# Optimization experiments

Hardware: AMD Instinct MI355X
Metric: run time of the kernel (lower is better)

Reference implementation:

```python
import jax, jax.numpy as jnp
from jax import lax
import numpy as np

N, I, H, B, T = 16, 128, 128, 32, 512  # n lstms, input_size, hidden_size, batch, seq_len


def setup_inputs() -> dict:
    key = jax.random.key(0)
    k0, k1, k2, k3, k4 = jax.random.split(key, 5)
    s = 1.0 / np.sqrt(H)  # PyTorch LSTM init scale U(-1/sqrt(H), 1/sqrt(H)); normal*s is fine numerically
    x = jax.random.normal(k0, (B, T, N * I), dtype=jnp.float32)
    W_ih = jax.random.normal(k1, (N, 4 * H, I), dtype=jnp.float32) * s
    W_hh = jax.random.normal(k2, (N, 4 * H, H), dtype=jnp.float32) * s
    b_ih = jax.random.normal(k3, (N, 4 * H), dtype=jnp.float32) * s
    b_hh = jax.random.normal(k4, (N, 4 * H), dtype=jnp.float32) * s
    return {"x": x, "W_ih": W_ih, "W_hh": W_hh, "b_ih": b_ih, "b_hh": b_hh}


def reference(x, W_ih, W_hh, b_ih, b_hh):
    """WideLSTM fused forward: N independent single-layer unidirectional LSTMs,
    hx=None (zero initial state), batch_first output [B, T, N*H], (h_n, c_n) [1, B, N*H].
    PyTorch gate order: i, f, g, o."""
    Bx, Tx, _ = x.shape
    n = W_ih.shape[0]
    h = W_hh.shape[-1]
    xs = x.reshape(Bx, Tx, n, -1).transpose(1, 0, 2, 3)  # [T, B, N, I]
    # Precompute input contribution + biases for all timesteps at once (one big GEMM)
    x_proj = jnp.einsum('tbni,ngi->tbng', xs, W_ih) + (b_ih + b_hh)  # [T, B, N, 4H]

    def step(carry, xp):
        hprev, cprev = carry
        z = xp + jnp.einsum('bnh,ngh->bng', hprev, W_hh)  # [B, N, 4H]
        i_g, f_g, g_g, o_g = jnp.split(z, 4, axis=-1)
        i_g = jax.nn.sigmoid(i_g)
        f_g = jax.nn.sigmoid(f_g)
        g_g = jnp.tanh(g_g)
        o_g = jax.nn.sigmoid(o_g)
        c = f_g * cprev + i_g * g_g
        hnew = o_g * jnp.tanh(c)
        return (hnew, c), hnew

    h0 = jnp.zeros((Bx, n, h), dtype=x.dtype)
    c0 = jnp.zeros((Bx, n, h), dtype=x.dtype)
    (h_n, c_n), hs = lax.scan(step, (h0, c0), x_proj)
    output = hs.transpose(1, 0, 2, 3).reshape(Bx, Tx, n * h)  # [B, T, N*H]
    h_n = h_n.reshape(1, Bx, n * h)  # [num_layers*num_dir=1, B, N*H]
    c_n = c_n.reshape(1, Bx, n * h)
    return output, h_n, c_n
```

## Files before the change

### kernel.cpp

```cpp
#include <hip/hip_runtime.h>

#define N_LSTM 16
#define ISZ 128
#define HSZ 128
#define BSZ 32
#define TSZ 512
#define G4H 512
#define XROW (N_LSTM * ISZ)
#define OROW (N_LSTM * HSZ)

typedef __attribute__((ext_vector_type(8))) short s16x8;
typedef __attribute__((ext_vector_type(4))) float f32x4;

#define LOG2E 1.4426950408889634f

static __device__ __forceinline__ unsigned short f2bf(float f) {
    unsigned int u = __builtin_bit_cast(unsigned int, f);
    u += 0x7fffu + ((u >> 16) & 1u);
    return (unsigned short)(u >> 16);
}

static __device__ __forceinline__ float fexp2(float x) {
#if __has_builtin(__builtin_amdgcn_exp2f)
    return __builtin_amdgcn_exp2f(x);
#else
    return __expf(x * 0.6931471805599453f);
#endif
}

static __device__ __forceinline__ void barrier_lgkm() {
    __builtin_amdgcn_sched_barrier(0);
    asm volatile("s_waitcnt lgkmcnt(0)" ::: "memory");
    __builtin_amdgcn_s_barrier();
    __builtin_amdgcn_sched_barrier(0);
}

__global__ void x_to_frag(const float* __restrict__ x, int4* __restrict__ xf) {
    const unsigned G = blockIdx.x * 256 + threadIdx.x;
    const int ln = G & 63;
    const int kt = (G >> 6) & 3;
    const int wg = (G >> 8) & 31;
    const int t  = G >> 13;
    const int lm = ln & 15, lq = ln >> 4;
    const int n  = wg >> 1;
    const int b0 = (wg & 1) * 16;
    const float* src = x + (size_t)(b0 + lm) * (TSZ * XROW) + (size_t)t * XROW
                         + n * ISZ + kt * 32 + lq * 8;
    float4 a = *(const float4*)src;
    float4 b = *(const float4*)(src + 4);
    s16x8 f;
    f[0] = (short)f2bf(a.x); f[1] = (short)f2bf(a.y);
    f[2] = (short)f2bf(a.z); f[3] = (short)f2bf(a.w);
    f[4] = (short)f2bf(b.x); f[5] = (short)f2bf(b.y);
    f[6] = (short)f2bf(b.z); f[7] = (short)f2bf(b.w);
    xf[G] = __builtin_bit_cast(int4, f);
}

template <int PRE>
__global__ __launch_bounds__(512, 2) void widelstm_fused(
    const float* __restrict__ x, const int4* __restrict__ xf,
    const float* __restrict__ Wih, const float* __restrict__ Whh,
    const float* __restrict__ bih, const float* __restrict__ bhh,
    float* __restrict__ out)
{
    __shared__ __align__(16) unsigned short xbuf[2][16][136];
    __shared__ __align__(16) unsigned short hbuf[2][16][136];

    const int tid = threadIdx.x;
    const int wv  = tid >> 6;
    const int ln  = tid & 63;
    const int lm  = ln & 15;
    const int lq  = ln >> 4;
    const int n    = blockIdx.x >> 1;
    const int half = blockIdx.x & 1;
    const int b0   = half * 16;
    const int grp = (wv ^ (wv >> 2)) & 1;

    const float gsc[4] = {-LOG2E, -LOG2E, -2.f * LOG2E, -LOG2E};
    s16x8 wih[4][4], whh[4][4];
    f32x4 biasv[4];
    #pragma unroll
    for (int g = 0; g < 4; ++g) {
        const int col = g * 128 + wv * 16 + lm;
        const float s = gsc[g];
        const float bb = (bih[n * G4H + col] + bhh[n * G4H + col]) * s;
        biasv[g] = (f32x4){bb, bb, bb, bb};
        #pragma unroll
        for (int kt = 0; kt < 4; ++kt) {
            const float* pi = Wih + ((size_t)n * G4H + col) * ISZ + kt * 32 + lq * 8;
            const float* ph = Whh + ((size_t)n * G4H + col) * HSZ + kt * 32 + lq * 8;
            s16x8 a, b;
            #pragma unroll
            for (int j = 0; j < 8; ++j) {
                a[j] = (short)f2bf(pi[j] * s);
                b[j] = (short)f2bf(ph[j] * s);
            }
            wih[g][kt] = a;
            whh[g][kt] = b;
        }
    }

    for (int i = tid; i < 16 * 136; i += 512)
        ((unsigned short*)hbuf[0])[i] = 0;

    const int sr = tid >> 5;
    const int sc = (tid & 31) * 4;
    const float* xrow = x + (size_t)(b0 + sr) * TSZ * XROW + n * ISZ + sc;
    const int4* xfb = xf + (size_t)blockIdx.x * 256 + ln;

    float4 xr;
    s16x8 xra, xrb, xrc, xrd;
    f32x4 xacc[4];

    if constexpr (PRE) {
        s16x8 c0 = __builtin_bit_cast(s16x8, xfb[0]);
        s16x8 c1 = __builtin_bit_cast(s16x8, xfb[64]);
        s16x8 c2 = __builtin_bit_cast(s16x8, xfb[128]);
        s16x8 c3 = __builtin_bit_cast(s16x8, xfb[192]);
        #pragma unroll
        for (int g = 0; g < 4; ++g)
            xacc[g] = __builtin_amdgcn_mfma_f32_16x16x32_bf16(c0, wih[g][0], biasv[g], 0, 0, 0);
        #pragma unroll
        for (int g = 0; g < 4; ++g)
            xacc[g] = __builtin_amdgcn_mfma_f32_16x16x32_bf16(c1, wih[g][1], xacc[g], 0, 0, 0);
        #pragma unroll
        for (int g = 0; g < 4; ++g)
            xacc[g] = __builtin_amdgcn_mfma_f32_16x16x32_bf16(c2, wih[g][2], xacc[g], 0, 0, 0);
        #pragma unroll
        for (int g = 0; g < 4; ++g)
            xacc[g] = __builtin_amdgcn_mfma_f32_16x16x32_bf16(c3, wih[g][3], xacc[g], 0, 0, 0);
        xra = __builtin_bit_cast(s16x8, xfb[8192]);
        xrb = __builtin_bit_cast(s16x8, xfb[8192 + 64]);
        xrc = __builtin_bit_cast(s16x8, xfb[8192 + 128]);
        xrd = __builtin_bit_cast(s16x8, xfb[8192 + 192]);
    } else {
        xr = *(const float4*)(xrow);
        unsigned int lo = (unsigned int)f2bf(xr.x) | ((unsigned int)f2bf(xr.y) << 16);
        unsigned int hi = (unsigned int)f2bf(xr.z) | ((unsigned int)f2bf(xr.w) << 16);
        *(uint2*)&xbuf[0][sr][sc] = make_uint2(lo, hi);
        barrier_lgkm();
        #pragma unroll
        for (int kt = 0; kt < 4; ++kt) {
            s16x8 axk = *(const s16x8*)&xbuf[0][lm][kt * 32 + lq * 8];
            #pragma unroll
            for (int g = 0; g < 4; ++g)
                xacc[g] = __builtin_amdgcn_mfma_f32_16x16x32_bf16(
                    axk, wih[g][kt], kt == 0 ? biasv[g] : xacc[g], 0, 0, 0);
        }
        xr = *(const float4*)(xrow + (size_t)XROW);
    }

    float cprev[4] = {0.f, 0.f, 0.f, 0.f};
    float hlast[4] = {0.f, 0.f, 0.f, 0.f};
    const int ocol = n * HSZ + wv * 16 + lm;

    float* po0 = out + (size_t)(b0 + lq * 4 + 0) * TSZ * OROW + ocol;
    float* po1 = out + (size_t)(b0 + lq * 4 + 1) * TSZ * OROW + ocol;
    float* po2 = out + (size_t)(b0 + lq * 4 + 2) * TSZ * OROW + ocol;
    float* po3 = out + (size_t)(b0 + lq * 4 + 3) * TSZ * OROW + ocol;

#define PH_X(T_)                                                                            \
    if ((T_) + 1 < TSZ) {                                                                   \
        _Pragma("unroll")                                                                   \
        for (int g = 0; g < 4; ++g)                                                         \
            xacc[g] = __builtin_amdgcn_mfma_f32_16x16x32_bf16(xra, wih[g][0], biasv[g], 0, 0, 0); \
        _Pragma("unroll")                                                                   \
        for (int g = 0; g < 4; ++g)                                                         \
            xacc[g] = __builtin_amdgcn_mfma_f32_16x16x32_bf16(xrb, wih[g][1], xacc[g], 0, 0, 0); \
        _Pragma("unroll")                                                                   \
        for (int g = 0; g < 4; ++g)                                                         \
            xacc[g] = __builtin_amdgcn_mfma_f32_16x16x32_bf16(xrc, wih[g][2], xacc[g], 0, 0, 0); \
        _Pragma("unroll")                                                                   \
        for (int g = 0; g < 4; ++g)                                                         \
            xacc[g] = __builtin_amdgcn_mfma_f32_16x16x32_bf16(xrd, wih[g][3], xacc[g], 0, 0, 0); \
        if ((T_) + 2 < TSZ) {                                                               \
            const int4* p = xfb + (size_t)((T_) + 2) * 8192;                                \
            xra = __builtin_bit_cast(s16x8, p[0]);                                          \
            xrb = __builtin_bit_cast(s16x8, p[64]);                                         \
            xrc = __builtin_bit_cast(s16x8, p[128]);                                        \
            xrd = __builtin_bit_cast(s16x8, p[192]);                                        \
        }                                                                                   \
    }

#define PH_EPI(NXT_)                                                                        \
    _Pragma("unroll")                                                                       \
    for (int r = 0; r < 4; ++r) {                                                           \
        float ei = fexp2(hacc[0][r]);                                                       \
        float ef = fexp2(hacc[1][r]);                                                       \
        float eg = fexp2(fminf(hacc[2][r], 80.f));                                          \
        float eo = fexp2(hacc[3][r]);                                                       \
        float fv = __builtin_amdgcn_rcpf(1.f + ef);                                         \
        float ig = (1.f - eg) * __builtin_amdgcn_rcpf((1.f + ei) * (1.f + eg));             \
        float c  = fv * cprev[r] + ig;                                                      \
        cprev[r] = c;                                                                       \
        float ec = fexp2(fminf(c * (-2.f * LOG2E), 80.f));                                  \
        float hv = (1.f - ec) * __builtin_amdgcn_rcpf((1.f + eo) * (1.f + ec));             \
        hlast[r] = hv;                                                                      \
        hbuf[NXT_][lq * 4 + r][wv * 16 + lm] = f2bf(hv);                                    \
        if (r == 0) { *po0 = hv; po0 += OROW; }                                             \
        if (r == 1) { *po1 = hv; po1 += OROW; }                                             \
        if (r == 2) { *po2 = hv; po2 += OROW; }                                             \
        if (r == 3) { *po3 = hv; po3 += OROW; }                                             \
    }

#define LSTM_STEP(T_, CUR_, NXT_)                                                           \
    {                                                                                       \
        const int t_ = (T_);                                                                \
        if constexpr (!PRE) {                                                               \
            if (t_ + 1 < TSZ) {                                                             \
                unsigned int lo = (unsigned int)f2bf(xr.x) | ((unsigned int)f2bf(xr.y) << 16); \
                unsigned int hi = (unsigned int)f2bf(xr.z) | ((unsigned int)f2bf(xr.w) << 16); \
                *(uint2*)&xbuf[NXT_][sr][sc] = make_uint2(lo, hi);                          \
            }                                                                               \
        }                                                                                   \
        barrier_lgkm();                  \
        s16x8 ah0 = *(const s16x8*)&hbuf[CUR_][lm][0 * 32 + lq * 8];                        \
        s16x8 ah1 = *(const s16x8*)&hbuf[CUR_][lm][1 * 32 + lq * 8];                        \
        s16x8 ah2 = *(const s16x8*)&hbuf[CUR_][lm][2 * 32 + lq * 8];                        \
        s16x8 ah3 = *(const s16x8*)&hbuf[CUR_][lm][3 * 32 + lq * 8];                        \
        if constexpr (!PRE) {                                                               \
            if (t_ + 2 < TSZ) xr = *(const float4*)(xrow + (size_t)(t_ + 2) * XROW);        \
        }                                                                                   \
        f32x4 hacc[4];                                                                      \
        _Pragma("unroll")                                                                   \
        for (int g = 0; g < 4; ++g)                                                         \
            hacc[g] = __builtin_amdgcn_mfma_f32_16x16x32_bf16(ah0, whh[g][0], xacc[g], 0, 0, 0); \
        _Pragma("unroll")                                                                   \
        for (int g = 0; g < 4; ++g)                                                         \
            hacc[g] = __builtin_amdgcn_mfma_f32_16x16x32_bf16(ah1, whh[g][1], hacc[g], 0, 0, 0); \
        _Pragma("unroll")                                                                   \
        for (int g = 0; g < 4; ++g)                                                         \
            hacc[g] = __builtin_amdgcn_mfma_f32_16x16x32_bf16(ah2, whh[g][2], hacc[g], 0, 0, 0); \
        _Pragma("unroll")                                                                   \
        for (int g = 0; g < 4; ++g)                                                         \
            hacc[g] = __builtin_amdgcn_mfma_f32_16x16x32_bf16(ah3, whh[g][3], hacc[g], 0, 0, 0); \
        if constexpr (PRE) {                                                                \
            if (grp == 0) {                                                                 \
                PH_X(t_);                                                                   \
                __builtin_amdgcn_sched_barrier(0);                                          \
                PH_EPI(NXT_);                                                               \
            } else {                                                                        \
                PH_EPI(NXT_);                                                               \
                __builtin_amdgcn_sched_barrier(0);                                          \
                PH_X(t_);                                                                   \
            }                                                                               \
        } else {                                                                            \
            if (t_ + 1 < TSZ) {                                                             \
                _Pragma("unroll")                                                           \
                for (int kt = 0; kt < 4; ++kt) {                                            \
                    s16x8 axk = *(const s16x8*)&xbuf[NXT_][lm][kt * 32 + lq * 8];           \
                    _Pragma("unroll")                                                       \
                    for (int g = 0; g < 4; ++g)                                             \
                        xacc[g] = __builtin_amdgcn_mfma_f32_16x16x32_bf16(                  \
                            axk, wih[g][kt], kt == 0 ? biasv[g] : xacc[g], 0, 0, 0);        \
                }                                                                           \
            }                                                                               \
            PH_EPI(NXT_);                                                                   \
        }                                                                                   \
    }

    for (int t = 0; t < TSZ; t += 2) {
        LSTM_STEP(t, 0, 1);
        LSTM_STEP(t + 1, 1, 0);
    }
#undef LSTM_STEP
#undef PH_X
#undef PH_EPI

    const size_t hn_off = (size_t)BSZ * TSZ * OROW;
    const size_t cn_off = hn_off + (size_t)BSZ * OROW;
    #pragma unroll
    for (int r = 0; r < 4; ++r) {
        const int row = lq * 4 + r;
        const size_t idx = (size_t)(b0 + row) * OROW + ocol;
        out[hn_off + idx] = hlast[r];
        out[cn_off + idx] = cprev[r];
    }
}

extern "C" void kernel_launch(void* const* d_in, const int* in_sizes, int n_in,
                              void* d_out, int out_size, void* d_ws, size_t ws_size,
                              hipStream_t stream) {
    const float* x   = (const float*)d_in[0];
    const float* Wih = (const float*)d_in[1];
    const float* Whh = (const float*)d_in[2];
    const float* bih = (const float*)d_in[3];
    const float* bhh = (const float*)d_in[4];
    float* out = (float*)d_out;

    const size_t need = (size_t)TSZ * 32 * 4 * 64 * 16;
    if (d_ws != nullptr && ws_size >= need) {
        int4* xfrag = (int4*)d_ws;
        x_to_frag<<<dim3(16384), dim3(256), 0, stream>>>(x, xfrag);
        widelstm_fused<1><<<dim3(32), dim3(512), 0, stream>>>(x, xfrag, Wih, Whh, bih, bhh, out);
    } else {
        widelstm_fused<0><<<dim3(32), dim3(512), 0, stream>>>(x, nullptr, Wih, Whh, bih, bhh, out);
    }
}
```

Baseline: 752.7 us.

## Precompute input projection in a parallel GEMM kernel before the recurrent scan

Adds an xp_gemm kernel that computes the input projection plus bias for all timesteps on a 32x8 grid and writes it in fp32 fragment layout to the workspace. A new recurrent kernel then only does the hidden-state MFMAs each step and prefetches the precomputed gate pre-activations two steps ahead. This takes the per-step W_ih MFMAs off the serial critical path, at the cost of a large fp32 workspace write and read (about 134 MB). The old fused kernel loses its wave-group phase staggering and remains as a fallback.

Measured after the change: 932.3 us. 1.24x slower.

```diff
diff --git a/kernel.cpp b/kernel.cpp
--- a/kernel.cpp
+++ b/kernel.cpp
@@ -33,6 +33,190 @@
     asm volatile("s_waitcnt lgkmcnt(0)" ::: "memory");
     __builtin_amdgcn_s_barrier();
     __builtin_amdgcn_sched_barrier(0);
+}
+
+__global__ __launch_bounds__(512, 2) void xp_gemm(
+    const float* __restrict__ x, const float* __restrict__ Wih,
+    const float* __restrict__ bih, const float* __restrict__ bhh,
+    float* __restrict__ xp)
+{
+    const int tid = threadIdx.x;
+    const int wv  = tid >> 6;
+    const int ln  = tid & 63;
+    const int lm  = ln & 15;
+    const int lq  = ln >> 4;
+    const int wg  = blockIdx.x;
+    const int tc  = blockIdx.y;
+    const int n   = wg >> 1;
+    const int b0  = (wg & 1) * 16;
+
+    const float gsc[4] = {-LOG2E, -LOG2E, -2.f * LOG2E, -LOG2E};
+    s16x8 wih[4][4];
+    f32x4 biasv[4];
+    #pragma unroll
+    for (int g = 0; g < 4; ++g) {
+        const int col = g * 128 + wv * 16 + lm;
+        const float s = gsc[g];
+        const float bb = (bih[n * G4H + col] + bhh[n * G4H + col]) * s;
+        biasv[g] = (f32x4){bb, bb, bb, bb};
+        #pragma unroll
+        for (int kt = 0; kt < 4; ++kt) {
+            const float* pi = Wih + ((size_t)n * G4H + col) * ISZ + kt * 32 + lq * 8;
+            s16x8 a;
+            #pragma unroll
+            for (int j = 0; j < 8; ++j) a[j] = (short)f2bf(pi[j] * s);
+            wih[g][kt] = a;
+        }
+    }
+
+    const float* xbase = x + (size_t)(b0 + lm) * (TSZ * XROW) + n * ISZ + lq * 8;
+    float* xpo = xp + (size_t)(wg * 8 + wv) * 1024 + ln * 4;
+
+    #pragma unroll 2
+    for (int tt = 0; tt < 64; ++tt) {
+        const int t = tc * 64 + tt;
+        const float* xr = xbase + (size_t)t * XROW;
+        s16x8 fr[4];
+        #pragma unroll
+        for (int kt = 0; kt < 4; ++kt) {
+            float4 a = *(const float4*)(xr + kt * 32);
+            float4 b = *(const float4*)(xr + kt * 32 + 4);
+            s16x8 f;
+            f[0] = (short)f2bf(a.x); f[1] = (short)f2bf(a.y);
+            f[2] = (short)f2bf(a.z); f[3] = (short)f2bf(a.w);
+            f[4] = (short)f2bf(b.x); f[5] = (short)f2bf(b.y);
+            f[6] = (short)f2bf(b.z); f[7] = (short)f2bf(b.w);
+            fr[kt] = f;
+        }
+        f32x4 acc[4];
+        #pragma unroll
+        for (int g = 0; g < 4; ++g) acc[g] = biasv[g];
+        #pragma unroll
+        for (int kt = 0; kt < 4; ++kt) {
+            #pragma unroll
+            for (int g = 0; g < 4; ++g)
+                acc[g] = __builtin_amdgcn_mfma_f32_16x16x32_bf16(fr[kt], wih[g][kt], acc[g], 0, 0, 0);
+        }
+        float* o = xpo + (size_t)t * 262144;
+        #pragma unroll
+        for (int g = 0; g < 4; ++g)
+            *(f32x4*)(o + g * 256) = acc[g];
+    }
+}
+
+__global__ __launch_bounds__(512, 2) void widelstm_rec_xp(
+    const float* __restrict__ xp, const float* __restrict__ Whh,
+    float* __restrict__ out)
+{
+    __shared__ __align__(16) unsigned short hbuf[2][16][136];
+
+    const int tid = threadIdx.x;
+    const int wv  = tid >> 6;
+    const int ln  = tid & 63;
+    const int lm  = ln & 15;
+    const int lq  = ln >> 4;
+    const int n    = blockIdx.x >> 1;
+    const int half = blockIdx.x & 1;
+    const int b0   = half * 16;
+
+    const float gsc[4] = {-LOG2E, -LOG2E, -2.f * LOG2E, -LOG2E};
+    s16x8 whh[4][4];
+    #pragma unroll
+    for (int g = 0; g < 4; ++g) {
+        const int col = g * 128 + wv * 16 + lm;
+        const float s = gsc[g];
+        #pragma unroll
+        for (int kt = 0; kt < 4; ++kt) {
+            const float* ph = Whh + ((size_t)n * G4H + col) * HSZ + kt * 32 + lq * 8;
+            s16x8 b;
+            #pragma unroll
+            for (int j = 0; j < 8; ++j) b[j] = (short)f2bf(ph[j] * s);
+            whh[g][kt] = b;
+        }
+    }
+
+    for (int i = tid; i < 16 * 136; i += 512)
+        ((unsigned short*)hbuf[0])[i] = 0;
+
+    const float* xq = xp + (size_t)(blockIdx.x * 8 + wv) * 1024 + ln * 4;
+
+    f32x4 pA[4], pB[4];
+    #pragma unroll
+    for (int g = 0; g < 4; ++g) pA[g] = *(const f32x4*)(xq + g * 256);
+    #pragma unroll
+    for (int g = 0; g < 4; ++g) pB[g] = *(const f32x4*)(xq + 262144 + g * 256);
+
+    float cprev[4] = {0.f, 0.f, 0.f, 0.f};
+    float hlast[4] = {0.f, 0.f, 0.f, 0.f};
+    const int ocol = n * HSZ + wv * 16 + lm;
+
+    float* po0 = out + (size_t)(b0 + lq * 4 + 0) * TSZ * OROW + ocol;
+    float* po1 = out + (size_t)(b0 + lq * 4 + 1) * TSZ * OROW + ocol;
+    float* po2 = out + (size_t)(b0 + lq * 4 + 2) * TSZ * OROW + ocol;
+    float* po3 = out + (size_t)(b0 + lq * 4 + 3) * TSZ * OROW + ocol;
+
+#define XP_STEP(T_, CUR_, NXT_, PC_, PN_)                                                   \
+    {                                                                                       \
+        const int t_ = (T_);                                                                \
+        barrier_lgkm();                                      \
+        s16x8 ah0 = *(const s16x8*)&hbuf[CUR_][lm][0 * 32 + lq * 8];                        \
+        s16x8 ah1 = *(const s16x8*)&hbuf[CUR_][lm][1 * 32 + lq * 8];                        \
+        s16x8 ah2 = *(const s16x8*)&hbuf[CUR_][lm][2 * 32 + lq * 8];                        \
+        s16x8 ah3 = *(const s16x8*)&hbuf[CUR_][lm][3 * 32 + lq * 8];                        \
+        f32x4 hacc[4];                                                                      \
+        _Pragma("unroll")                                                                   \
+        for (int g = 0; g < 4; ++g)                                                         \
+            hacc[g] = __builtin_amdgcn_mfma_f32_16x16x32_bf16(ah0, whh[g][0], PC_[g], 0, 0, 0); \
+        _Pragma("unroll")                                                                   \
+        for (int g = 0; g < 4; ++g)                                                         \
+            hacc[g] = __builtin_amdgcn_mfma_f32_16x16x32_bf16(ah1, whh[g][1], hacc[g], 0, 0, 0); \
+        _Pragma("unroll")                                                                   \
+        for (int g = 0; g < 4; ++g)                                                         \
+            hacc[g] = __builtin_amdgcn_mfma_f32_16x16x32_bf16(ah2, whh[g][2], hacc[g], 0, 0, 0); \
+        _Pragma("unroll")                                                                   \
+        for (int g = 0; g < 4; ++g)                                                         \
+            hacc[g] = __builtin_amdgcn_mfma_f32_16x16x32_bf16(ah3, whh[g][3], hacc[g], 0, 0, 0); \
+        if (t_ + 2 < TSZ) {               \
+            const float* p = xq + (size_t)(t_ + 2) * 262144;                                \
+            _Pragma("unroll")                                                               \
+            for (int g = 0; g < 4; ++g) PC_[g] = *(const f32x4*)(p + g * 256);              \
+        }                                                                                   \
+        _Pragma("unroll")                                                                   \
+        for (int r = 0; r < 4; ++r) {                                                       \
+            float ei = fexp2(hacc[0][r]);                                                   \
+            float ef = fexp2(hacc[1][r]);                                                   \
+            float eg = fexp2(fminf(hacc[2][r], 80.f));                                      \
+            float eo = fexp2(hacc[3][r]);                                                   \
+            float fv = __builtin_amdgcn_rcpf(1.f + ef);                                     \
+            float ig = (1.f - eg) * __builtin_amdgcn_rcpf((1.f + ei) * (1.f + eg));         \
+            float c  = fv * cprev[r] + ig;                                                  \
+            cprev[r] = c;                                                                   \
+            float ec = fexp2(fminf(c * (-2.f * LOG2E), 80.f));                              \
+            float hv = (1.f - ec) * __builtin_amdgcn_rcpf((1.f + eo) * (1.f + ec));         \
+            hlast[r] = hv;                                                                  \
+            hbuf[NXT_][lq * 4 + r][wv * 16 + lm] = f2bf(hv);                                \
+            if (r == 0) { *po0 = hv; po0 += OROW; }                                         \
+            if (r == 1) { *po1 = hv; po1 += OROW; }                                         \
+            if (r == 2) { *po2 = hv; po2 += OROW; }                                         \
+            if (r == 3) { *po3 = hv; po3 += OROW; }                                         \
+        }                                                                                   \
+    }
+
+    for (int t = 0; t < TSZ; t += 2) {
+        XP_STEP(t, 0, 1, pA, pB);
+        XP_STEP(t + 1, 1, 0, pB, pA);
+    }
+#undef XP_STEP
+
+    const size_t hn_off = (size_t)BSZ * TSZ * OROW;
+    const size_t cn_off = hn_off + (size_t)BSZ * OROW;
+    #pragma unroll
+    for (int r = 0; r < 4; ++r) {
+        const int row = lq * 4 + r;
+        const size_t idx = (size_t)(b0 + row) * OROW + ocol;
+        out[hn_off + idx] = hlast[r];
+        out[cn_off + idx] = cprev[r];
+    }
 }
 
 __global__ void x_to_frag(const float* __restrict__ x, int4* __restrict__ xf) {
@@ -74,7 +258,6 @@
     const int n    = blockIdx.x >> 1;
     const int half = blockIdx.x & 1;
     const int b0   = half * 16;
-    const int grp = (wv ^ (wv >> 2)) & 1;
 
     const float gsc[4] = {-LOG2E, -LOG2E, -2.f * LOG2E, -LOG2E};
     s16x8 wih[4][4], whh[4][4];
@@ -159,50 +342,6 @@
     float* po2 = out + (size_t)(b0 + lq * 4 + 2) * TSZ * OROW + ocol;
     float* po3 = out + (size_t)(b0 + lq * 4 + 3) * TSZ * OROW + ocol;
 
-#define PH_X(T_)                                                                            \
-    if ((T_) + 1 < TSZ) {                                                                   \
-        _Pragma("unroll")                                                                   \
-        for (int g = 0; g < 4; ++g)                                                         \
-            xacc[g] = __builtin_amdgcn_mfma_f32_16x16x32_bf16(xra, wih[g][0], biasv[g], 0, 0, 0); \
-        _Pragma("unroll")                                                                   \
-        for (int g = 0; g < 4; ++g)                                                         \
-            xacc[g] = __builtin_amdgcn_mfma_f32_16x16x32_bf16(xrb, wih[g][1], xacc[g], 0, 0, 0); \
-        _Pragma("unroll")                                                                   \
-        for (int g = 0; g < 4; ++g)                                                         \
-            xacc[g] = __builtin_amdgcn_mfma_f32_16x16x32_bf16(xrc, wih[g][2], xacc[g], 0, 0, 0); \
-        _Pragma("unroll")                                                                   \
-        for (int g = 0; g < 4; ++g)                                                         \
-            xacc[g] = __builtin_amdgcn_mfma_f32_16x16x32_bf16(xrd, wih[g][3], xacc[g], 0, 0, 0); \
-        if ((T_) + 2 < TSZ) {                                                               \
-            const int4* p = xfb + (size_t)((T_) + 2) * 8192;                                \
-            xra = __builtin_bit_cast(s16x8, p[0]);                                          \
-            xrb = __builtin_bit_cast(s16x8, p[64]);                                         \
-            xrc = __builtin_bit_cast(s16x8, p[128]);                                        \
-            xrd = __builtin_bit_cast(s16x8, p[192]);                                        \
-        }                                                                                   \
-    }
-
-#define PH_EPI(NXT_)                                                                        \
-    _Pragma("unroll")                                                                       \
-    for (int r = 0; r < 4; ++r) {                                                           \
-        float ei = fexp2(hacc[0][r]);                                                       \
-        float ef = fexp2(hacc[1][r]);                                                       \
-        float eg = fexp2(fminf(hacc[2][r], 80.f));                                          \
-        float eo = fexp2(hacc[3][r]);                                                       \
-        float fv = __builtin_amdgcn_rcpf(1.f + ef);                                         \
-        float ig = (1.f - eg) * __builtin_amdgcn_rcpf((1.f + ei) * (1.f + eg));             \
-        float c  = fv * cprev[r] + ig;                                                      \
-        cprev[r] = c;                                                                       \
-        float ec = fexp2(fminf(c * (-2.f * LOG2E), 80.f));                                  \
-        float hv = (1.f - ec) * __builtin_amdgcn_rcpf((1.f + eo) * (1.f + ec));             \
-        hlast[r] = hv;                                                                      \
-        hbuf[NXT_][lq * 4 + r][wv * 16 + lm] = f2bf(hv);                                    \
-        if (r == 0) { *po0 = hv; po0 += OROW; }                                             \
-        if (r == 1) { *po1 = hv; po1 += OROW; }                                             \
-        if (r == 2) { *po2 = hv; po2 += OROW; }                                             \
-        if (r == 3) { *po3 = hv; po3 += OROW; }                                             \
-    }
-
 #define LSTM_STEP(T_, CUR_, NXT_)                                                           \
     {                                                                                       \
         const int t_ = (T_);                                                                \
@@ -213,7 +352,7 @@
                 *(uint2*)&xbuf[NXT_][sr][sc] = make_uint2(lo, hi);                          \
             }                                                                               \
         }                                                                                   \
-        barrier_lgkm();                  \
+        barrier_lgkm();                                                                     \
         s16x8 ah0 = *(const s16x8*)&hbuf[CUR_][lm][0 * 32 + lq * 8];                        \
         s16x8 ah1 = *(const s16x8*)&hbuf[CUR_][lm][1 * 32 + lq * 8];                        \
         s16x8 ah2 = *(const s16x8*)&hbuf[CUR_][lm][2 * 32 + lq * 8];                        \
@@ -234,18 +373,28 @@
         _Pragma("unroll")                                                                   \
         for (int g = 0; g < 4; ++g)                                                         \
             hacc[g] = __builtin_amdgcn_mfma_f32_16x16x32_bf16(ah3, whh[g][3], hacc[g], 0, 0, 0); \
-        if constexpr (PRE) {                                                                \
-            if (grp == 0) {                                                                 \
-                PH_X(t_);                                                                   \
-                __builtin_amdgcn_sched_barrier(0);                                          \
-                PH_EPI(NXT_);                                                               \
+        if (t_ + 1 < TSZ) {                                                                 \
+            if constexpr (PRE) {                                                            \
+                _Pragma("unroll")                                                           \
+                for (int g = 0; g < 4; ++g)                                                 \
+                    xacc[g] = __builtin_amdgcn_mfma_f32_16x16x32_bf16(xra, wih[g][0], biasv[g], 0, 0, 0); \
+                _Pragma("unroll")                                                           \
+                for (int g = 0; g < 4; ++g)                                                 \
+                    xacc[g] = __builtin_amdgcn_mfma_f32_16x16x32_bf16(xrb, wih[g][1], xacc[g], 0, 0, 0); \
+                _Pragma("unroll")                                                           \
+                for (int g = 0; g < 4; ++g)                                                 \
+                    xacc[g] = __builtin_amdgcn_mfma_f32_16x16x32_bf16(xrc, wih[g][2], xacc[g], 0, 0, 0); \
+                _Pragma("unroll")                                                           \
+                for (int g = 0; g < 4; ++g)                                                 \
+                    xacc[g] = __builtin_amdgcn_mfma_f32_16x16x32_bf16(xrd, wih[g][3], xacc[g], 0, 0, 0); \
+                if (t_ + 2 < TSZ) {                                                         \
+                    const int4* p = xfb + (size_t)(t_ + 2) * 8192;                          \
+                    xra = __builtin_bit_cast(s16x8, p[0]);                                  \
+                    xrb = __builtin_bit_cast(s16x8, p[64]);                                 \
+                    xrc = __builtin_bit_cast(s16x8, p[128]);                                \
+                    xrd = __builtin_bit_cast(s16x8, p[192]);                                \
+                }                                                                           \
             } else {                                                                        \
-                PH_EPI(NXT_);                                                               \
-                __builtin_amdgcn_sched_barrier(0);                                          \
-                PH_X(t_);                                                                   \
-            }                                                                               \
-        } else {                                                                            \
-            if (t_ + 1 < TSZ) {                                                             \
                 _Pragma("unroll")                                                           \
                 for (int kt = 0; kt < 4; ++kt) {                                            \
                     s16x8 axk = *(const s16x8*)&xbuf[NXT_][lm][kt * 32 + lq * 8];           \
@@ -255,7 +404,25 @@
                             axk, wih[g][kt], kt == 0 ? biasv[g] : xacc[g], 0, 0, 0);        \
                 }                                                                           \
             }                                                                               \
-            PH_EPI(NXT_);                                                                   \
+        }                                                                                   \
+        _Pragma("unroll")                                                                   \
+        for (int r = 0; r < 4; ++r) {                                                       \
+            float ei = fexp2(hacc[0][r]);                                                   \
+            float ef = fexp2(hacc[1][r]);                                                   \
+            float eg = fexp2(fminf(hacc[2][r], 80.f));                                      \
+            float eo = fexp2(hacc[3][r]);                                                   \
+            float fv = __builtin_amdgcn_rcpf(1.f + ef);                                     \
+            float ig = (1.f - eg) * __builtin_amdgcn_rcpf((1.f + ei) * (1.f + eg));         \
+            float c  = fv * cprev[r] + ig;                                                  \
+            cprev[r] = c;                                                                   \
+            float ec = fexp2(fminf(c * (-2.f * LOG2E), 80.f));                              \
+            float hv = (1.f - ec) * __builtin_amdgcn_rcpf((1.f + eo) * (1.f + ec));         \
+            hlast[r] = hv;                                                                  \
+            hbuf[NXT_][lq * 4 + r][wv * 16 + lm] = f2bf(hv);                                \
+            if (r == 0) { *po0 = hv; po0 += OROW; }                                         \
+            if (r == 1) { *po1 = hv; po1 += OROW; }                                         \
+            if (r == 2) { *po2 = hv; po2 += OROW; }                                         \
+            if (r == 3) { *po3 = hv; po3 += OROW; }                                         \
         }                                                                                   \
     }
 
@@ -264,8 +431,6 @@
         LSTM_STEP(t + 1, 1, 0);
     }
 #undef LSTM_STEP
-#undef PH_X
-#undef PH_EPI
 
     const size_t hn_off = (size_t)BSZ * TSZ * OROW;
     const size_t cn_off = hn_off + (size_t)BSZ * OROW;
@@ -288,8 +453,13 @@
     const float* bhh = (const float*)d_in[4];
     float* out = (float*)d_out;
 
-    const size_t need = (size_t)TSZ * 32 * 4 * 64 * 16;
-    if (d_ws != nullptr && ws_size >= need) {
+    const size_t needXP = (size_t)TSZ * 32 * 8 * 4 * 256 * 4;
+    const size_t needFR = (size_t)TSZ * 32 * 4 * 64 * 16;
+    if (d_ws != nullptr && ws_size >= needXP) {
+        float* xp = (float*)d_ws;
+        xp_gemm<<<dim3(32, 8), dim3(512), 0, stream>>>(x, Wih, bih, bhh, xp);
+        widelstm_rec_xp<<<dim3(32), dim3(512), 0, stream>>>(xp, Whh, out);
+    } else if (d_ws != nullptr && ws_size >= needFR) {
         int4* xfrag = (int4*)d_ws;
         x_to_frag<<<dim3(16384), dim3(256), 0, stream>>>(x, xfrag);
         widelstm_fused<1><<<dim3(32), dim3(512), 0, stream>>>(x, xfrag, Wih, Whh, bih, bhh, out);
```

## Double-buffer input-projection accumulators and issue next-step x MFMAs before recurrent MFMAs

Applied to the files above, without the earlier changes.

The recurrent step now computes the next timestep's input projection into a second accumulator set (ping-pong xaccA/xaccB) before the h·W_hh MFMAs. This replaces the wave-group split that ordered x-projection and epilogue differently per wave. The goal is to fill the MFMA pipe while waiting on the h dependency chain. The epilogue is reformulated to use one reciprocal for the cell update instead of two. Launch bounds drop to 1 block per CU, which gives more registers at the cost of occupancy hints.

Result: faster. 726.6 us (-3.5%).

```diff
diff --git a/kernel.cpp b/kernel.cpp
--- a/kernel.cpp
+++ b/kernel.cpp
@@ -57,7 +57,7 @@
 }
 
 template <int PRE>
-__global__ __launch_bounds__(512, 2) void widelstm_fused(
+__global__ __launch_bounds__(512, 1) void widelstm_fused(
     const float* __restrict__ x, const int4* __restrict__ xf,
     const float* __restrict__ Wih, const float* __restrict__ Whh,
     const float* __restrict__ bih, const float* __restrict__ bhh,
@@ -74,7 +74,6 @@
     const int n    = blockIdx.x >> 1;
     const int half = blockIdx.x & 1;
     const int b0   = half * 16;
-    const int grp = (wv ^ (wv >> 2)) & 1;
 
     const float gsc[4] = {-LOG2E, -LOG2E, -2.f * LOG2E, -LOG2E};
     s16x8 wih[4][4], whh[4][4];
@@ -110,7 +109,7 @@
 
     float4 xr;
     s16x8 xra, xrb, xrc, xrd;
-    f32x4 xacc[4];
+    f32x4 xaccA[4], xaccB[4];
 
     if constexpr (PRE) {
         s16x8 c0 = __builtin_bit_cast(s16x8, xfb[0]);
@@ -119,16 +118,16 @@
         s16x8 c3 = __builtin_bit_cast(s16x8, xfb[192]);
         #pragma unroll
         for (int g = 0; g < 4; ++g)
-            xacc[g] = __builtin_amdgcn_mfma_f32_16x16x32_bf16(c0, wih[g][0], biasv[g], 0, 0, 0);
+            xaccA[g] = __builtin_amdgcn_mfma_f32_16x16x32_bf16(c0, wih[g][0], biasv[g], 0, 0, 0);
         #pragma unroll
         for (int g = 0; g < 4; ++g)
-            xacc[g] = __builtin_amdgcn_mfma_f32_16x16x32_bf16(c1, wih[g][1], xacc[g], 0, 0, 0);
+            xaccA[g] = __builtin_amdgcn_mfma_f32_16x16x32_bf16(c1, wih[g][1], xaccA[g], 0, 0, 0);
         #pragma unroll
         for (int g = 0; g < 4; ++g)
-            xacc[g] = __builtin_amdgcn_mfma_f32_16x16x32_bf16(c2, wih[g][2], xacc[g], 0, 0, 0);
+            xaccA[g] = __builtin_amdgcn_mfma_f32_16x16x32_bf16(c2, wih[g][2], xaccA[g], 0, 0, 0);
         #pragma unroll
         for (int g = 0; g < 4; ++g)
-            xacc[g] = __builtin_amdgcn_mfma_f32_16x16x32_bf16(c3, wih[g][3], xacc[g], 0, 0, 0);
+            xaccA[g] = __builtin_amdgcn_mfma_f32_16x16x32_bf16(c3, wih[g][3], xaccA[g], 0, 0, 0);
         xra = __builtin_bit_cast(s16x8, xfb[8192]);
         xrb = __builtin_bit_cast(s16x8, xfb[8192 + 64]);
         xrc = __builtin_bit_cast(s16x8, xfb[8192 + 128]);
@@ -144,8 +143,8 @@
             s16x8 axk = *(const s16x8*)&xbuf[0][lm][kt * 32 + lq * 8];
             #pragma unroll
             for (int g = 0; g < 4; ++g)
-                xacc[g] = __builtin_amdgcn_mfma_f32_16x16x32_bf16(
-                    axk, wih[g][kt], kt == 0 ? biasv[g] : xacc[g], 0, 0, 0);
+                xaccA[g] = __builtin_amdgcn_mfma_f32_16x16x32_bf16(
+                    axk, wih[g][kt], kt == 0 ? biasv[g] : xaccA[g], 0, 0, 0);
         }
         xr = *(const float4*)(xrow + (size_t)XROW);
     }
@@ -158,29 +157,6 @@
     float* po1 = out + (size_t)(b0 + lq * 4 + 1) * TSZ * OROW + ocol;
     float* po2 = out + (size_t)(b0 + lq * 4 + 2) * TSZ * OROW + ocol;
     float* po3 = out + (size_t)(b0 + lq * 4 + 3) * TSZ * OROW + ocol;
-
-#define PH_X(T_)                                                                            \
-    if ((T_) + 1 < TSZ) {                                                                   \
-        _Pragma("unroll")                                                                   \
-        for (int g = 0; g < 4; ++g)                                                         \
-            xacc[g] = __builtin_amdgcn_mfma_f32_16x16x32_bf16(xra, wih[g][0], biasv[g], 0, 0, 0); \
-        _Pragma("unroll")                                                                   \
-        for (int g = 0; g < 4; ++g)                                                         \
-            xacc[g] = __builtin_amdgcn_mfma_f32_16x16x32_bf16(xrb, wih[g][1], xacc[g], 0, 0, 0); \
-        _Pragma("unroll")                                                                   \
-        for (int g = 0; g < 4; ++g)                                                         \
-            xacc[g] = __builtin_amdgcn_mfma_f32_16x16x32_bf16(xrc, wih[g][2], xacc[g], 0, 0, 0); \
-        _Pragma("unroll")                                                                   \
-        for (int g = 0; g < 4; ++g)                                                         \
-            xacc[g] = __builtin_amdgcn_mfma_f32_16x16x32_bf16(xrd, wih[g][3], xacc[g], 0, 0, 0); \
-        if ((T_) + 2 < TSZ) {                                                               \
-            const int4* p = xfb + (size_t)((T_) + 2) * 8192;                                \
-            xra = __builtin_bit_cast(s16x8, p[0]);                                          \
-            xrb = __builtin_bit_cast(s16x8, p[64]);                                         \
-            xrc = __builtin_bit_cast(s16x8, p[128]);                                        \
-            xrd = __builtin_bit_cast(s16x8, p[192]);                                        \
-        }                                                                                   \
-    }
 
 #define PH_EPI(NXT_)                                                                        \
     _Pragma("unroll")                                                                       \
@@ -189,9 +165,10 @@
         float ef = fexp2(hacc[1][r]);                                                       \
         float eg = fexp2(fminf(hacc[2][r], 80.f));                                          \
         float eo = fexp2(hacc[3][r]);                                                       \
-        float fv = __builtin_amdgcn_rcpf(1.f + ef);                                         \
-        float ig = (1.f - eg) * __builtin_amdgcn_rcpf((1.f + ei) * (1.f + eg));             \
-        float c  = fv * cprev[r] + ig;                                                      \
+        float af = 1.f + ef;                                                                \
+        float p1 = (1.f + ei) * (1.f + eg);                                                 \
+        float num = cprev[r] * p1 + (1.f - eg) * af;                                        \
+        float c   = num * __builtin_amdgcn_rcpf(af * p1);                                   \
         cprev[r] = c;                                                                       \
         float ec = fexp2(fminf(c * (-2.f * LOG2E), 80.f));                                  \
         float hv = (1.f - ec) * __builtin_amdgcn_rcpf((1.f + eo) * (1.f + ec));             \
@@ -203,28 +180,40 @@
         if (r == 3) { *po3 = hv; po3 += OROW; }                                             \
     }
 
-#define LSTM_STEP(T_, CUR_, NXT_)                                                           \
+    if constexpr (PRE) {
+#define STEP_P(T_, CUR_, NXT_, XC_, XN_)                                                    \
     {                                                                                       \
         const int t_ = (T_);                                                                \
-        if constexpr (!PRE) {                                                               \
-            if (t_ + 1 < TSZ) {                                                             \
-                unsigned int lo = (unsigned int)f2bf(xr.x) | ((unsigned int)f2bf(xr.y) << 16); \
-                unsigned int hi = (unsigned int)f2bf(xr.z) | ((unsigned int)f2bf(xr.w) << 16); \
-                *(uint2*)&xbuf[NXT_][sr][sc] = make_uint2(lo, hi);                          \
-            }                                                                               \
-        }                                                                                   \
-        barrier_lgkm();                  \
+        barrier_lgkm();                                      \
         s16x8 ah0 = *(const s16x8*)&hbuf[CUR_][lm][0 * 32 + lq * 8];                        \
         s16x8 ah1 = *(const s16x8*)&hbuf[CUR_][lm][1 * 32 + lq * 8];                        \
         s16x8 ah2 = *(const s16x8*)&hbuf[CUR_][lm][2 * 32 + lq * 8];                        \
         s16x8 ah3 = *(const s16x8*)&hbuf[CUR_][lm][3 * 32 + lq * 8];                        \
-        if constexpr (!PRE) {                                                               \
-            if (t_ + 2 < TSZ) xr = *(const float4*)(xrow + (size_t)(t_ + 2) * XROW);        \
+        if (t_ + 1 < TSZ) {               \
+            _Pragma("unroll")                                                               \
+            for (int g = 0; g < 4; ++g)                                                     \
+                XN_[g] = __builtin_amdgcn_mfma_f32_16x16x32_bf16(xra, wih[g][0], biasv[g], 0, 0, 0); \
+            _Pragma("unroll")                                                               \
+            for (int g = 0; g < 4; ++g)                                                     \
+                XN_[g] = __builtin_amdgcn_mfma_f32_16x16x32_bf16(xrb, wih[g][1], XN_[g], 0, 0, 0); \
+            _Pragma("unroll")                                                               \
+            for (int g = 0; g < 4; ++g)                                                     \
+                XN_[g] = __builtin_amdgcn_mfma_f32_16x16x32_bf16(xrc, wih[g][2], XN_[g], 0, 0, 0); \
+            _Pragma("unroll")                                                               \
+            for (int g = 0; g < 4; ++g)                                                     \
+                XN_[g] = __builtin_amdgcn_mfma_f32_16x16x32_bf16(xrd, wih[g][3], XN_[g], 0, 0, 0); \
+            if (t_ + 2 < TSZ) {                                 \
+                const int4* p = xfb + (size_t)(t_ + 2) * 8192;                              \
+                xra = __builtin_bit_cast(s16x8, p[0]);                                      \
+                xrb = __builtin_bit_cast(s16x8, p[64]);                                     \
+                xrc = __builtin_bit_cast(s16x8, p[128]);                                    \
+                xrd = __builtin_bit_cast(s16x8, p[192]);                                    \
+            }                                                                               \
         }                                                                                   \
         f32x4 hacc[4];                                                                      \
         _Pragma("unroll")                                                                   \
         for (int g = 0; g < 4; ++g)                                                         \
-            hacc[g] = __builtin_amdgcn_mfma_f32_16x16x32_bf16(ah0, whh[g][0], xacc[g], 0, 0, 0); \
+            hacc[g] = __builtin_amdgcn_mfma_f32_16x16x32_bf16(ah0, whh[g][0], XC_[g], 0, 0, 0); \
         _Pragma("unroll")                                                                   \
         for (int g = 0; g < 4; ++g)                                                         \
             hacc[g] = __builtin_amdgcn_mfma_f32_16x16x32_bf16(ah1, whh[g][1], hacc[g], 0, 0, 0); \
@@ -234,37 +223,61 @@
         _Pragma("unroll")                                                                   \
         for (int g = 0; g < 4; ++g)                                                         \
             hacc[g] = __builtin_amdgcn_mfma_f32_16x16x32_bf16(ah3, whh[g][3], hacc[g], 0, 0, 0); \
-        if constexpr (PRE) {                                                                \
-            if (grp == 0) {                                                                 \
-                PH_X(t_);                                                                   \
-                __builtin_amdgcn_sched_barrier(0);                                          \
-                PH_EPI(NXT_);                                                               \
-            } else {                                                                        \
-                PH_EPI(NXT_);                                                               \
-                __builtin_amdgcn_sched_barrier(0);                                          \
-                PH_X(t_);                                                                   \
+        PH_EPI(NXT_);                                                                       \
+    }
+
+        for (int t = 0; t < TSZ; t += 2) {
+            STEP_P(t, 0, 1, xaccA, xaccB);
+            STEP_P(t + 1, 1, 0, xaccB, xaccA);
+        }
+#undef STEP_P
+    } else {
+#define STEP_0(T_, CUR_, NXT_)                                                              \
+    {                                                                                       \
+        const int t_ = (T_);                                                                \
+        if (t_ + 1 < TSZ) {                                                                 \
+            unsigned int lo = (unsigned int)f2bf(xr.x) | ((unsigned int)f2bf(xr.y) << 16);  \
+            unsigned int hi = (unsigned int)f2bf(xr.z) | ((unsigned int)f2bf(xr.w) << 16);  \
+            *(uint2*)&xbuf[NXT_][sr][sc] = make_uint2(lo, hi);                              \
+        }                                                                                   \
+        barrier_lgkm();                                                                     \
+        s16x8 ah0 = *(const s16x8*)&hbuf[CUR_][lm][0 * 32 + lq * 8];                        \
+        s16x8 ah1 = *(const s16x8*)&hbuf[CUR_][lm][1 * 32 + lq * 8];                        \
+        s16x8 ah2 = *(const s16x8*)&hbuf[CUR_][lm][2 * 32 + lq * 8];                        \
+        s16x8 ah3 = *(const s16x8*)&hbuf[CUR_][lm][3 * 32 + lq * 8];                        \
+        if (t_ + 2 < TSZ) xr = *(const float4*)(xrow + (size_t)(t_ + 2) * XROW);            \
+        f32x4 hacc[4];                                                                      \
+        _Pragma("unroll")                                                                   \
+        for (int g = 0; g < 4; ++g)                                                         \
+            hacc[g] = __builtin_amdgcn_mfma_f32_16x16x32_bf16(ah0, whh[g][0], xaccA[g], 0, 0, 0); \
+        _Pragma("unroll")                                                                   \
+        for (int g = 0; g < 4; ++g)                                                         \
+            hacc[g] = __builtin_amdgcn_mfma_f32_16x16x32_bf16(ah1, whh[g][1], hacc[g], 0, 0, 0); \
+        _Pragma("unroll")                                                                   \
+        for (int g = 0; g < 4; ++g)                                                         \
+            hacc[g] = __builtin_amdgcn_mfma_f32_16x16x32_bf16(ah2, whh[g][2], hacc[g], 0, 0, 0); \
+        _Pragma("unroll")                                                                   \
+        for (int g = 0; g < 4; ++g)                                                         \
+            hacc[g] = __builtin_amdgcn_mfma_f32_16x16x32_bf16(ah3, whh[g][3], hacc[g], 0, 0, 0); \
+        if (t_ + 1 < TSZ) {                                                                 \
+            _Pragma("unroll")                                                               \
+            for (int kt = 0; kt < 4; ++kt) {                                                \
+                s16x8 axk = *(const s16x8*)&xbuf[NXT_][lm][kt * 32 + lq * 8];               \
+                _Pragma("unroll")                                                           \
+                for (int g = 0; g < 4; ++g)                                                 \
+                    xaccA[g] = __builtin_amdgcn_mfma_f32_16x16x32_bf16(                     \
+                        axk, wih[g][kt], kt == 0 ? biasv[g] : xaccA[g], 0, 0, 0);           \
             }                                                                               \
-        } else {                                                                            \
-            if (t_ + 1 < TSZ) {                                                             \
-                _Pragma("unroll")                                                           \
-                for (int kt = 0; kt < 4; ++kt) {                                            \
-                    s16x8 axk = *(const s16x8*)&xbuf[NXT_][lm][kt * 32 + lq * 8];           \
-                    _Pragma("unroll")                                                       \
-                    for (int g = 0; g < 4; ++g)                                             \
-                        xacc[g] = __builtin_amdgcn_mfma_f32_16x16x32_bf16(                  \
-                            axk, wih[g][kt], kt == 0 ? biasv[g] : xacc[g], 0, 0, 0);        \
-                }                                                                           \
-            }                                                                               \
-            PH_EPI(NXT_);                                                                   \
         }                                                                                   \
-    }
-
-    for (int t = 0; t < TSZ; t += 2) {
-        LSTM_STEP(t, 0, 1);
-        LSTM_STEP(t + 1, 1, 0);
-    }
-#undef LSTM_STEP
-#undef PH_X
+        PH_EPI(NXT_);                                                                       \
+    }
+
+        for (int t = 0; t < TSZ; t += 2) {
+            STEP_0(t, 0, 1);
+            STEP_0(t + 1, 1, 0);
+        }
+#undef STEP_0
+    }
 #undef PH_EPI
 
     const size_t hn_off = (size_t)BSZ * TSZ * OROW;
@@ -288,8 +301,8 @@
     const float* bhh = (const float*)d_in[4];
     float* out = (float*)d_out;
 
-    const size_t need = (size_t)TSZ * 32 * 4 * 64 * 16;
-    if (d_ws != nullptr && ws_size >= need) {
+    const size_t needFR = (size_t)TSZ * 32 * 4 * 64 * 16;
+    if (d_ws != nullptr && ws_size >= needFR) {
         int4* xfrag = (int4*)d_ws;
         x_to_frag<<<dim3(16384), dim3(256), 0, stream>>>(x, xfrag);
         widelstm_fused<1><<<dim3(32), dim3(512), 0, stream>>>(x, xfrag, Wih, Whh, bih, bhh, out);
```
